# Performance work log

Measured on AMD Instinct MI355X. Metric: run time of the kernel, lower is better.

The kernel has to match this reference:

```python
import jax, jax.numpy as jnp
import numpy as np

B, S, HID = 2, 2048, 1024
H, KVH, D = 16, 4, 64
N_REP = H // KVH
SCALE = D ** -0.5
CAP = 50.0


def rotate_half(x):
    x1, x2 = x[..., : D // 2], x[..., D // 2 :]
    return jnp.concatenate((-x2, x1), axis=-1)


def setup_inputs() -> dict:
    key = jax.random.key(0)
    ks = jax.random.split(key, 10)
    X = jax.random.normal(ks[0], (B, S, HID), dtype=jnp.float32)
    # RoPE tables: (B, S, D)
    inv_freq = 1.0 / (10000.0 ** (np.arange(0, D, 2, dtype=np.float32) / D))
    pos = np.arange(S, dtype=np.float32)
    freqs = np.outer(pos, inv_freq)  # (S, D/2)
    emb = np.concatenate([freqs, freqs], axis=-1)  # (S, D)
    cos = jnp.broadcast_to(jnp.asarray(np.cos(emb)), (B, S, D))
    sin = jnp.broadcast_to(jnp.asarray(np.sin(emb)), (B, S, D))
    # causal mask: 1 where key <= query
    mask = jnp.broadcast_to(jnp.tril(jnp.ones((S, S), dtype=jnp.int32)), (B, S, S))
    std = HID ** -0.5
    Wq = jax.random.normal(ks[1], (HID, HID), dtype=jnp.float32) * std
    bq = jnp.zeros((HID,), dtype=jnp.float32)
    Wk = jax.random.normal(ks[2], (KVH * D, HID), dtype=jnp.float32) * std
    bk = jnp.zeros((KVH * D,), dtype=jnp.float32)
    Wv = jax.random.normal(ks[3], (KVH * D, HID), dtype=jnp.float32) * std
    bv = jnp.zeros((KVH * D,), dtype=jnp.float32)
    Wo = jax.random.normal(ks[4], (HID, HID), dtype=jnp.float32) * std
    bo = jnp.zeros((HID,), dtype=jnp.float32)
    return {"X": X, "cos": cos, "sin": sin, "mask": mask,
            "Wq": Wq, "bq": bq, "Wk": Wk, "bk": bk,
            "Wv": Wv, "bv": bv, "Wo": Wo, "bo": bo}


def reference(X, cos, sin, mask, Wq, bq, Wk, bk, Wv, bv, Wo, bo):
    bsz, q_len, _ = X.shape
    q = (X @ Wq.T + bq).reshape(bsz, q_len, H, D).transpose(0, 2, 1, 3)    # (B,H,S,D)
    k = (X @ Wk.T + bk).reshape(bsz, q_len, KVH, D).transpose(0, 2, 1, 3)  # (B,KVH,S,D)
    v = (X @ Wv.T + bv).reshape(bsz, q_len, KVH, D).transpose(0, 2, 1, 3)
    c = cos[:, None, :, :]  # (B,1,S,D)
    s = sin[:, None, :, :]
    q = q * c + rotate_half(q) * s
    k = k * c + rotate_half(k) * s
    k = jnp.repeat(k, N_REP, axis=1)  # GQA expand -> (B,H,S,D)
    v = jnp.repeat(v, N_REP, axis=1)
    scores = jnp.einsum('bhqd,bhkd->bhqk', q, k) * SCALE
    scores = jnp.clip(scores, -CAP, CAP)  # attention cap
    scores = jnp.where(mask[:, None, :, :] == 0, -1e9, scores)
    attn = jax.nn.softmax(scores, axis=-1)  # dropout p=0 -> identity
    ctx = jnp.einsum('bhqk,bhkd->bhqd', attn, v)
    ctx = ctx.transpose(0, 2, 1, 3).reshape(bsz, q_len, H * D)
    out = ctx @ Wo.T + bo
    return (out, attn)
```

## Files before the change

### kernel.cpp

```cpp
#include <hip/hip_runtime.h>
#include <cstdint>
#include <cstddef>

#define S_LEN   2048
#define BATCH   2
#define HID_DIM 1024
#define NHEAD   16
#define NKV     4
#define DHEAD   64
#define SCALE_F 0.125f
#define CAP_F   50.0f
#define L2E     1.44269504f

typedef unsigned short u16;
typedef __attribute__((ext_vector_type(8))) short  short8_t;
typedef __attribute__((ext_vector_type(4))) float  f32x4;
typedef __attribute__((ext_vector_type(4))) u16    u16x4;

static __device__ __forceinline__ u16 f2bf(float f) {
  uint32_t x = __builtin_bit_cast(uint32_t, f);
  x += 0x7fffu + ((x >> 16) & 1u);
  return (u16)(x >> 16);
}

static __device__ __forceinline__ void gload_lds16(const void* g, void* l) {
  __builtin_amdgcn_global_load_lds((const __attribute__((address_space(1))) void*)g,
                                   (__attribute__((address_space(3))) void*)l, 16, 0, 0);
}

static __device__ __forceinline__ float expclamp(float x) {
  float c = __builtin_amdgcn_fmed3f(x, -CAP_F, CAP_F);
  return __builtin_amdgcn_exp2f(c * L2E - CAP_F * L2E);
}

__global__ void cast_all(const float* __restrict__ X,  u16* __restrict__ xb,
                         const float* __restrict__ Wq, u16* __restrict__ wqb,
                         const float* __restrict__ Wk, u16* __restrict__ wkb,
                         const float* __restrict__ Wv, u16* __restrict__ wvb,
                         const float* __restrict__ Wo, u16* __restrict__ wob) {
  const float* src; u16* dst; int n4;
  switch (blockIdx.y) {
    case 0:  src = X;  dst = xb;  n4 = (BATCH * S_LEN * HID_DIM) / 4; break;
    case 1:  src = Wq; dst = wqb; n4 = (HID_DIM * HID_DIM) / 4;       break;
    case 2:  src = Wk; dst = wkb; n4 = (NKV * DHEAD * HID_DIM) / 4;   break;
    case 3:  src = Wv; dst = wvb; n4 = (NKV * DHEAD * HID_DIM) / 4;   break;
    default: src = Wo; dst = wob; n4 = (HID_DIM * HID_DIM) / 4;       break;
  }
  for (int i = blockIdx.x * 256 + threadIdx.x; i < n4; i += gridDim.x * 256) {
    f32x4 v = ((const f32x4*)src)[i];
    u16x4 o;
    o[0] = f2bf(v[0]); o[1] = f2bf(v[1]); o[2] = f2bf(v[2]); o[3] = f2bf(v[3]);
    ((u16x4*)dst)[i] = o;
  }
}

__global__ __launch_bounds__(256) void gemm_qkv(const u16* __restrict__ Xb,
                                                const u16* __restrict__ Wqb,
                                                const u16* __restrict__ Wkb,
                                                const u16* __restrict__ Wvb,
                                                const float* __restrict__ bq,
                                                const float* __restrict__ bk,
                                                const float* __restrict__ bv,
                                                const float* __restrict__ cosb,
                                                const float* __restrict__ sinb,
                                                u16* __restrict__ qout,
                                                u16* __restrict__ kout,
                                                u16* __restrict__ vtout) {
  __shared__ u16 As[128 * 64];
  __shared__ u16 Bs[128 * 64];
  const int tid = threadIdx.x, lane = tid & 63, wid = tid >> 6;
  const int l15 = lane & 15, lg = lane >> 4;
  const int m0 = blockIdx.x * 128, n0 = blockIdx.y * 128;
  const int wm = wid & 1, wn = wid >> 1;
  const int K = HID_DIM;

  const u16* Wp; const float* biasp; int nl, mode;
  if (n0 < 1024)      { Wp = Wqb; biasp = bq; nl = n0;        mode = 0; }
  else if (n0 < 1280) { Wp = Wkb; biasp = bk; nl = n0 - 1024; mode = 1; }
  else                { Wp = Wvb; biasp = bv; nl = n0 - 1280; mode = 2; }

  f32x4 acc[4][4];
  #pragma unroll
  for (int a = 0; a < 4; ++a)
    #pragma unroll
    for (int b2 = 0; b2 < 4; ++b2) acc[a][b2] = (f32x4){0.f, 0.f, 0.f, 0.f};

  const int srow = (lane >> 3), sg = (lane & 7);

  for (int kk = 0; kk < K; kk += 64) {
    __syncthreads();
    #pragma unroll
    for (int i = 0; i < 4; ++i) {
      const int c = wid * 4 + i;
      const int r = c * 8 + srow;
      const int g = sg ^ (r & 7);
      gload_lds16(Xb + (size_t)(m0 + r) * K + kk + g * 8, As + c * 512);
      gload_lds16(Wp + (size_t)(nl + r) * K + kk + g * 8, Bs + c * 512);
    }
    __syncthreads();
    #pragma unroll
    for (int ks = 0; ks < 2; ++ks) {
      short8_t xa[4], wb[4];
      #pragma unroll
      for (int f = 0; f < 4; ++f) {
        const int rm = wm * 64 + f * 16 + l15;
        const int rn = wn * 64 + f * 16 + l15;
        xa[f] = *(const short8_t*)(As + rm * 64 + (((ks * 4 + lg) ^ (rm & 7)) * 8));
        wb[f] = *(const short8_t*)(Bs + rn * 64 + (((ks * 4 + lg) ^ (rn & 7)) * 8));
      }
      if (mode != 2) {
        #pragma unroll
        for (int fn = 0; fn < 4; ++fn)
          #pragma unroll
          for (int fm = 0; fm < 4; ++fm)
            acc[fn][fm] = __builtin_amdgcn_mfma_f32_16x16x32_bf16(wb[fn], xa[fm], acc[fn][fm], 0, 0, 0);
      } else {
        #pragma unroll
        for (int fn = 0; fn < 4; ++fn)
          #pragma unroll
          for (int fm = 0; fm < 4; ++fm)
            acc[fn][fm] = __builtin_amdgcn_mfma_f32_16x16x32_bf16(xa[fm], wb[fn], acc[fn][fm], 0, 0, 0);
      }
    }
  }

  const int m_base = m0 + wm * 64;
  const int nlb = nl + wn * 64;

  if (mode < 2) {
    const int Nout = (mode == 0) ? HID_DIM : (NKV * DHEAD);
    u16* outb = (mode == 0) ? qout : kout;
    #pragma unroll
    for (int fm = 0; fm < 4; ++fm) {
      const int row = m_base + fm * 16 + l15;
      #pragma unroll
      for (int fn = 0; fn < 2; ++fn) {
        const int dh = fn * 16 + lg * 4;
        const f32x4 c4 = *(const f32x4*)(cosb + (size_t)row * 64 + dh);
        const f32x4 s4 = *(const f32x4*)(sinb + (size_t)row * 64 + dh);
        f32x4 x1 = acc[fn][fm]     + *(const f32x4*)(biasp + nlb + fn * 16 + lg * 4);
        f32x4 x2 = acc[fn + 2][fm] + *(const f32x4*)(biasp + nlb + (fn + 2) * 16 + lg * 4);
        f32x4 o1 = x1 * c4 - x2 * s4;
        f32x4 o2 = x2 * c4 + x1 * s4;
        u16x4 u1, u2;
        #pragma unroll
        for (int i = 0; i < 4; ++i) { u1[i] = f2bf(o1[i]); u2[i] = f2bf(o2[i]); }
        *(u16x4*)(outb + (size_t)row * Nout + nlb + fn * 16 + lg * 4)       = u1;
        *(u16x4*)(outb + (size_t)row * Nout + nlb + (fn + 2) * 16 + lg * 4) = u2;
      }
    }
  } else {
    #pragma unroll
    for (int fn = 0; fn < 4; ++fn) {
      const int d = nlb + fn * 16 + l15;
      const float bvs = biasp[d];
      #pragma unroll
      for (int fm = 0; fm < 4; ++fm) {
        const int s0 = m_base + fm * 16 + lg * 4;
        const int b_ = s0 >> 11, s_ = s0 & (S_LEN - 1);
        u16x4 o;
        #pragma unroll
        for (int i = 0; i < 4; ++i) o[i] = f2bf(acc[fn][fm][i] + bvs);
        *(u16x4*)(vtout + (size_t)(b_ * 256 + d) * S_LEN + s_) = o;
      }
    }
  }
}

__global__ __launch_bounds__(256) void gemm_out(const u16* __restrict__ A,
                                                const u16* __restrict__ W,
                                                const float* __restrict__ bias,
                                                float* __restrict__ outp) {
  __shared__ u16 As[128 * 64];
  __shared__ u16 Bs[128 * 64];
  const int tid = threadIdx.x, lane = tid & 63, wid = tid >> 6;
  const int l15 = lane & 15, lg = lane >> 4;
  const int m0 = blockIdx.x * 128, n0 = blockIdx.y * 128;
  const int wm = wid & 1, wn = wid >> 1;
  const int K = HID_DIM, N = HID_DIM;

  f32x4 acc[4][4];
  #pragma unroll
  for (int a = 0; a < 4; ++a)
    #pragma unroll
    for (int b2 = 0; b2 < 4; ++b2) acc[a][b2] = (f32x4){0.f, 0.f, 0.f, 0.f};

  const int srow = (lane >> 3), sg = (lane & 7);

  for (int kk = 0; kk < K; kk += 64) {
    __syncthreads();
    #pragma unroll
    for (int i = 0; i < 4; ++i) {
      const int c = wid * 4 + i;
      const int r = c * 8 + srow;
      const int g = sg ^ (r & 7);
      gload_lds16(A + (size_t)(m0 + r) * K + kk + g * 8, As + c * 512);
      gload_lds16(W + (size_t)(n0 + r) * K + kk + g * 8, Bs + c * 512);
    }
    __syncthreads();
    #pragma unroll
    for (int ks = 0; ks < 2; ++ks) {
      short8_t xa[4], wb[4];
      #pragma unroll
      for (int f = 0; f < 4; ++f) {
        const int rm = wm * 64 + f * 16 + l15;
        const int rn = wn * 64 + f * 16 + l15;
        xa[f] = *(const short8_t*)(As + rm * 64 + (((ks * 4 + lg) ^ (rm & 7)) * 8));
        wb[f] = *(const short8_t*)(Bs + rn * 64 + (((ks * 4 + lg) ^ (rn & 7)) * 8));
      }
      #pragma unroll
      for (int fn = 0; fn < 4; ++fn)
        #pragma unroll
        for (int fm = 0; fm < 4; ++fm)
          acc[fn][fm] = __builtin_amdgcn_mfma_f32_16x16x32_bf16(wb[fn], xa[fm], acc[fn][fm], 0, 0, 0);
    }
  }

  const int m_base = m0 + wm * 64, n_base = n0 + wn * 64;
  #pragma unroll
  for (int fn = 0; fn < 4; ++fn) {
    const int col = n_base + fn * 16 + lg * 4;
    const f32x4 bvv = *(const f32x4*)(bias + col);
    #pragma unroll
    for (int fm = 0; fm < 4; ++fm) {
      const int row = m_base + fm * 16 + l15;
      *(f32x4*)(outp + (size_t)row * N + col) = acc[fn][fm] + bvv;
    }
  }
}

__global__ __launch_bounds__(512) void attn_fused(const u16* __restrict__ qb,
                                                  const u16* __restrict__ kb,
                                                  const u16* __restrict__ vtb,
                                                  float* __restrict__ attn,
                                                  u16* __restrict__ ctxb) {
  __shared__ u16 kS[2][64 * 64];
  __shared__ u16 vS[2][64 * 64];
  __shared__ u16 pS[8][16][72];

  const int tid = threadIdx.x, lane = tid & 63, wid = tid >> 6;
  const int l15 = lane & 15, lg = lane >> 4;
  const int bh = blockIdx.x, b = bh >> 4, h = bh & 15, kvh = h >> 2;
  const int qt = (int)(gridDim.y - 1 - blockIdx.y);
  const int q0 = qt * 128;
  const int NT = 2 * qt + 2;
  const int qw = q0 + wid * 16;
  const int qrow = qw + l15;

  const u16* qp = qb + (size_t)(b * S_LEN + qrow) * HID_DIM + h * DHEAD + lg * 8;
  const short8_t qf0 = *(const short8_t*)qp;
  const short8_t qf1 = *(const short8_t*)(qp + 32);

  const u16* kbase  = kb  + (size_t)(b * S_LEN) * (NKV * DHEAD) + kvh * DHEAD;
  const u16* vtbase = vtb + (size_t)(b * NKV + kvh) * DHEAD * S_LEN;

  const int sr = tid >> 3;
  const int sg = (tid & 7) ^ (sr & 7);

  auto stageK = [&](int bi, int kv0) {
    gload_lds16(kbase + (size_t)(kv0 + sr) * (NKV * DHEAD) + sg * 8, &kS[bi][tid * 8]);
  };
  auto stageV = [&](int bi, int kv0) {
    gload_lds16(vtbase + (size_t)sr * S_LEN + kv0 + sg * 8, &vS[bi][tid * 8]);
  };

  float lsum = 0.f;
  stageK(0, 0);
  for (int t = 0; t < NT; ++t) {
    const int kv0 = t * 64;
    if (t + 1 < NT) {
      stageK((t + 1) & 1, kv0 + 64);
      asm volatile("s_waitcnt vmcnt(1)" ::: "memory");
    } else {
      asm volatile("s_waitcnt vmcnt(0)" ::: "memory");
    }
    __builtin_amdgcn_s_barrier();
    if (kv0 <= qw + 15) {
      const u16* ks = kS[t & 1];
      const bool maskc = (kv0 + 63 > qw);
      #pragma unroll
      for (int g16 = 0; g16 < 4; ++g16) {
        const int r = g16 * 16 + l15;
        short8_t ka0 = *(const short8_t*)(ks + r * 64 + ((lg ^ (r & 7)) * 8));
        short8_t ka1 = *(const short8_t*)(ks + r * 64 + (((4 + lg) ^ (r & 7)) * 8));
        f32x4 sacc = (f32x4){0.f, 0.f, 0.f, 0.f};
        sacc = __builtin_amdgcn_mfma_f32_16x16x32_bf16(ka0, qf0, sacc, 0, 0, 0);
        sacc = __builtin_amdgcn_mfma_f32_16x16x32_bf16(ka1, qf1, sacc, 0, 0, 0);
        #pragma unroll
        for (int i = 0; i < 4; ++i) {
          float e = expclamp(sacc[i] * SCALE_F);
          if (maskc) {
            const int kvi = kv0 + g16 * 16 + lg * 4 + i;
            e = (kvi <= qrow) ? e : 0.f;
          }
          lsum += e;
        }
      }
    }
    __builtin_amdgcn_s_barrier();
  }
  lsum += __shfl_xor(lsum, 16);
  lsum += __shfl_xor(lsum, 32);
  const float invl = 1.f / lsum;

  float* abase = attn + (size_t)bh * S_LEN * S_LEN;
  float* arow  = abase + (size_t)qrow * S_LEN;
  f32x4 ctx[4];
  #pragma unroll
  for (int dt = 0; dt < 4; ++dt) ctx[dt] = (f32x4){0.f, 0.f, 0.f, 0.f};

  stageK(0, 0);
  stageV(0, 0);
  for (int t = 0; t < NT; ++t) {
    const int kv0 = t * 64;
    if (t + 1 < NT) {
      stageK((t + 1) & 1, kv0 + 64);
      stageV((t + 1) & 1, kv0 + 64);
      asm volatile("s_waitcnt vmcnt(2)" ::: "memory");
    } else {
      asm volatile("s_waitcnt vmcnt(0)" ::: "memory");
    }
    __builtin_amdgcn_s_barrier();
    if (kv0 > qw + 15) {
      const f32x4 z = (f32x4){0.f, 0.f, 0.f, 0.f};
      #pragma unroll
      for (int g16 = 0; g16 < 4; ++g16)
        *(f32x4*)(arow + kv0 + g16 * 16 + lg * 4) = z;
    } else {
      const u16* ks = kS[t & 1];
      const u16* vs = vS[t & 1];
      const bool maskc = (kv0 + 63 > qw);
      #pragma unroll
      for (int g16 = 0; g16 < 4; ++g16) {
        const int r = g16 * 16 + l15;
        short8_t ka0 = *(const short8_t*)(ks + r * 64 + ((lg ^ (r & 7)) * 8));
        short8_t ka1 = *(const short8_t*)(ks + r * 64 + (((4 + lg) ^ (r & 7)) * 8));
        f32x4 sacc = (f32x4){0.f, 0.f, 0.f, 0.f};
        sacc = __builtin_amdgcn_mfma_f32_16x16x32_bf16(ka0, qf0, sacc, 0, 0, 0);
        sacc = __builtin_amdgcn_mfma_f32_16x16x32_bf16(ka1, qf1, sacc, 0, 0, 0);
        f32x4 pv; u16x4 pb;
        #pragma unroll
        for (int i = 0; i < 4; ++i) {
          float e = expclamp(sacc[i] * SCALE_F);
          if (maskc) {
            const int kvi = kv0 + g16 * 16 + lg * 4 + i;
            e = (kvi <= qrow) ? e : 0.f;
          }
          float p = e * invl;
          pv[i] = p;
          pb[i] = f2bf(p);
        }
        *(f32x4*)(arow + kv0 + g16 * 16 + lg * 4) = pv;
        *(u16x4*)&pS[wid][l15][g16 * 16 + lg * 4] = pb;
      }
      short8_t pa0 = *(const short8_t*)&pS[wid][l15][lg * 8];
      short8_t pa1 = *(const short8_t*)&pS[wid][l15][32 + lg * 8];
      #pragma unroll
      for (int dt = 0; dt < 4; ++dt) {
        const int r = dt * 16 + l15;
        short8_t bv0 = *(const short8_t*)(vs + r * 64 + ((lg ^ (r & 7)) * 8));
        short8_t bv1 = *(const short8_t*)(vs + r * 64 + (((4 + lg) ^ (r & 7)) * 8));
        ctx[dt] = __builtin_amdgcn_mfma_f32_16x16x32_bf16(bv0, pa0, ctx[dt], 0, 0, 0);
        ctx[dt] = __builtin_amdgcn_mfma_f32_16x16x32_bf16(bv1, pa1, ctx[dt], 0, 0, 0);
      }
    }
    __builtin_amdgcn_s_barrier();
  }

  #pragma unroll
  for (int dt = 0; dt < 4; ++dt) {
    u16x4 o;
    #pragma unroll
    for (int i = 0; i < 4; ++i) o[i] = f2bf(ctx[dt][i]);
    *(u16x4*)(ctxb + (size_t)(b * S_LEN + qrow) * HID_DIM + h * DHEAD + dt * 16 + lg * 4) = o;
  }

  const int zc0 = q0 + 128;
  if (zc0 < S_LEN) {
    const f32x4 z = (f32x4){0.f, 0.f, 0.f, 0.f};
    for (int r = wid; r < 128; r += 8) {
      float* rowp = abase + (size_t)(q0 + r) * S_LEN;
      for (int c = zc0 + lane * 4; c < S_LEN; c += 256)
        *(f32x4*)(rowp + c) = z;
    }
  }
}

extern "C" void kernel_launch(void* const* d_in, const int* in_sizes, int n_in,
                              void* d_out, int out_size, void* d_ws, size_t ws_size,
                              hipStream_t stream) {
  (void)in_sizes; (void)n_in; (void)out_size; (void)ws_size;
  const float* X    = (const float*)d_in[0];
  const float* cosb = (const float*)d_in[1];
  const float* sinb = (const float*)d_in[2];
  const float* Wq = (const float*)d_in[4];
  const float* bq = (const float*)d_in[5];
  const float* Wk = (const float*)d_in[6];
  const float* bk = (const float*)d_in[7];
  const float* Wv = (const float*)d_in[8];
  const float* bv = (const float*)d_in[9];
  const float* Wo = (const float*)d_in[10];
  const float* bo = (const float*)d_in[11];

  float* outp  = (float*)d_out;
  float* attnp = outp + (size_t)BATCH * S_LEN * HID_DIM;

  const int M = BATCH * S_LEN;
  u16* ws    = (u16*)d_ws;
  u16* Xb    = ws;
  u16* Wqb   = Xb  + (size_t)M * HID_DIM;
  u16* Wkb   = Wqb + (size_t)HID_DIM * HID_DIM;
  u16* Wvb   = Wkb + (size_t)NKV * DHEAD * HID_DIM;
  u16* Wob   = Wvb + (size_t)NKV * DHEAD * HID_DIM;
  u16* qbuf  = Wob + (size_t)HID_DIM * HID_DIM;
  u16* kbuf  = qbuf + (size_t)M * HID_DIM;
  u16* vtbuf = kbuf + (size_t)M * NKV * DHEAD;
  u16* ctxb  = vtbuf + (size_t)M * NKV * DHEAD;

  cast_all<<<dim3(1024, 5), 256, 0, stream>>>(X, Xb, Wq, Wqb, Wk, Wkb, Wv, Wvb, Wo, Wob);

  gemm_qkv<<<dim3(M / 128, 12), 256, 0, stream>>>(Xb, Wqb, Wkb, Wvb, bq, bk, bv,
                                                  cosb, sinb, qbuf, kbuf, vtbuf);

  attn_fused<<<dim3(BATCH * NHEAD, S_LEN / 128), 512, 0, stream>>>(qbuf, kbuf, vtbuf, attnp, ctxb);

  gemm_out<<<dim3(M / 128, HID_DIM / 128), 256, 0, stream>>>(ctxb, Wob, bo, outp);
}
```

Measured before the change: 229.7 us.

## Shrink attention tiles to 64 queries, regroup blocks by KV head, fold scale into Q

The attention kernel now uses 256-thread blocks, each covering 64 query rows, launched as a 1D grid of 1024. The grid is ordered so the four query heads sharing a KV head are adjacent, with heavy causal tiles scheduled first, to improve K/V cache reuse and load balance. Because each warp now always has work, the causal skip branches are removed. The softmax scale and log2e factor are folded into Q in the QKV GEMM epilogue, so the exp path needs only a clamp and subtract, though rounding Q to bf16 after scaling slightly changes numerics. Probability and zero-fill stores to the attention matrix use nontemporal stores, and the row sum is kept in four separate accumulators.

```diff
diff --git a/kernel.cpp b/kernel.cpp
--- a/kernel.cpp
+++ b/kernel.cpp
@@ -9,8 +9,9 @@
 #define NKV     4
 #define DHEAD   64
 #define SCALE_F 0.125f
-#define CAP_F   50.0f
 #define L2E     1.44269504f
+#define QSCALE  (SCALE_F * L2E)
+#define CAPL2   (50.0f * L2E)
 
 typedef unsigned short u16;
 typedef __attribute__((ext_vector_type(8))) short  short8_t;
@@ -28,9 +29,8 @@
                                    (__attribute__((address_space(3))) void*)l, 16, 0, 0);
 }
 
-static __device__ __forceinline__ float expclamp(float x) {
-  float c = __builtin_amdgcn_fmed3f(x, -CAP_F, CAP_F);
-  return __builtin_amdgcn_exp2f(c * L2E - CAP_F * L2E);
+static __device__ __forceinline__ float expclamp2(float x) {
+  return __builtin_amdgcn_exp2f(__builtin_amdgcn_fmed3f(x, -CAPL2, CAPL2) - CAPL2);
 }
 
 __global__ void cast_all(const float* __restrict__ X,  u16* __restrict__ xb,
@@ -129,6 +129,7 @@
 
   if (mode < 2) {
     const int Nout = (mode == 0) ? HID_DIM : (NKV * DHEAD);
+    const float qs = (mode == 0) ? QSCALE : 1.0f;
     u16* outb = (mode == 0) ? qout : kout;
     #pragma unroll
     for (int fm = 0; fm < 4; ++fm) {
@@ -140,8 +141,8 @@
         const f32x4 s4 = *(const f32x4*)(sinb + (size_t)row * 64 + dh);
         f32x4 x1 = acc[fn][fm]     + *(const f32x4*)(biasp + nlb + fn * 16 + lg * 4);
         f32x4 x2 = acc[fn + 2][fm] + *(const f32x4*)(biasp + nlb + (fn + 2) * 16 + lg * 4);
-        f32x4 o1 = x1 * c4 - x2 * s4;
-        f32x4 o2 = x2 * c4 + x1 * s4;
+        f32x4 o1 = (x1 * c4 - x2 * s4) * qs;
+        f32x4 o2 = (x2 * c4 + x1 * s4) * qs;
         u16x4 u1, u2;
         #pragma unroll
         for (int i = 0; i < 4; ++i) { u1[i] = f2bf(o1[i]); u2[i] = f2bf(o2[i]); }
@@ -229,21 +230,28 @@
   }
 }
 
-__global__ __launch_bounds__(512) void attn_fused(const u16* __restrict__ qb,
+__global__ __launch_bounds__(256) void attn_fused(const u16* __restrict__ qb,
                                                   const u16* __restrict__ kb,
                                                   const u16* __restrict__ vtb,
                                                   float* __restrict__ attn,
                                                   u16* __restrict__ ctxb) {
   __shared__ u16 kS[2][64 * 64];
   __shared__ u16 vS[2][64 * 64];
-  __shared__ u16 pS[8][16][72];
+  __shared__ u16 pS[4][16][72];
 
   const int tid = threadIdx.x, lane = tid & 63, wid = tid >> 6;
   const int l15 = lane & 15, lg = lane >> 4;
-  const int bh = blockIdx.x, b = bh >> 4, h = bh & 15, kvh = h >> 2;
-  const int qt = (int)(gridDim.y - 1 - blockIdx.y);
-  const int q0 = qt * 128;
-  const int NT = 2 * qt + 2;
+
+  const int lin = blockIdx.x;
+  const int g8  = lin & 7;
+  const int rem = lin >> 3;
+  const int h2  = rem & 3;
+  const int qt  = 31 - (rem >> 2);
+  const int b   = g8 >> 2, kvh = g8 & 3, h = kvh * 4 + h2;
+  const int bh  = b * 16 + h;
+
+  const int q0 = qt * 64;
+  const int NT = qt + 1;
   const int qw = q0 + wid * 16;
   const int qrow = qw + l15;
 
@@ -254,51 +262,62 @@
   const u16* kbase  = kb  + (size_t)(b * S_LEN) * (NKV * DHEAD) + kvh * DHEAD;
   const u16* vtbase = vtb + (size_t)(b * NKV + kvh) * DHEAD * S_LEN;
 
-  const int sr = tid >> 3;
-  const int sg = (tid & 7) ^ (sr & 7);
+  const int sr8 = wid * 8 + (lane >> 3);
+  const int sgr = lane & 7;
 
   auto stageK = [&](int bi, int kv0) {
-    gload_lds16(kbase + (size_t)(kv0 + sr) * (NKV * DHEAD) + sg * 8, &kS[bi][tid * 8]);
+    #pragma unroll
+    for (int it = 0; it < 2; ++it) {
+      const int r = it * 32 + sr8;
+      const int g = sgr ^ (r & 7);
+      gload_lds16(kbase + (size_t)(kv0 + r) * (NKV * DHEAD) + g * 8,
+                  &kS[bi][(it * 32 + wid * 8) * 64]);
+    }
   };
   auto stageV = [&](int bi, int kv0) {
-    gload_lds16(vtbase + (size_t)sr * S_LEN + kv0 + sg * 8, &vS[bi][tid * 8]);
+    #pragma unroll
+    for (int it = 0; it < 2; ++it) {
+      const int r = it * 32 + sr8;
+      const int g = sgr ^ (r & 7);
+      gload_lds16(vtbase + (size_t)r * S_LEN + kv0 + g * 8,
+                  &vS[bi][(it * 32 + wid * 8) * 64]);
+    }
   };
 
-  float lsum = 0.f;
+  f32x4 lacc = (f32x4){0.f, 0.f, 0.f, 0.f};
   stageK(0, 0);
   for (int t = 0; t < NT; ++t) {
     const int kv0 = t * 64;
     if (t + 1 < NT) {
       stageK((t + 1) & 1, kv0 + 64);
-      asm volatile("s_waitcnt vmcnt(1)" ::: "memory");
+      asm volatile("s_waitcnt vmcnt(2)" ::: "memory");
     } else {
       asm volatile("s_waitcnt vmcnt(0)" ::: "memory");
     }
     __builtin_amdgcn_s_barrier();
-    if (kv0 <= qw + 15) {
-      const u16* ks = kS[t & 1];
-      const bool maskc = (kv0 + 63 > qw);
-      #pragma unroll
-      for (int g16 = 0; g16 < 4; ++g16) {
-        const int r = g16 * 16 + l15;
-        short8_t ka0 = *(const short8_t*)(ks + r * 64 + ((lg ^ (r & 7)) * 8));
-        short8_t ka1 = *(const short8_t*)(ks + r * 64 + (((4 + lg) ^ (r & 7)) * 8));
-        f32x4 sacc = (f32x4){0.f, 0.f, 0.f, 0.f};
-        sacc = __builtin_amdgcn_mfma_f32_16x16x32_bf16(ka0, qf0, sacc, 0, 0, 0);
-        sacc = __builtin_amdgcn_mfma_f32_16x16x32_bf16(ka1, qf1, sacc, 0, 0, 0);
-        #pragma unroll
-        for (int i = 0; i < 4; ++i) {
-          float e = expclamp(sacc[i] * SCALE_F);
-          if (maskc) {
-            const int kvi = kv0 + g16 * 16 + lg * 4 + i;
-            e = (kvi <= qrow) ? e : 0.f;
-          }
-          lsum += e;
+    const u16* ks = kS[t & 1];
+    const bool maskc = (kv0 + 63 > qw);
+    #pragma unroll
+    for (int g16 = 0; g16 < 4; ++g16) {
+      const int r = g16 * 16 + l15;
+      short8_t ka0 = *(const short8_t*)(ks + r * 64 + ((lg ^ (r & 7)) * 8));
+      short8_t ka1 = *(const short8_t*)(ks + r * 64 + (((4 + lg) ^ (r & 7)) * 8));
+      f32x4 sacc = (f32x4){0.f, 0.f, 0.f, 0.f};
+      sacc = __builtin_amdgcn_mfma_f32_16x16x32_bf16(ka0, qf0, sacc, 0, 0, 0);
+      sacc = __builtin_amdgcn_mfma_f32_16x16x32_bf16(ka1, qf1, sacc, 0, 0, 0);
+      #pragma unroll
+      for (int i = 0; i < 4; ++i) {
+        float e = expclamp2(sacc[i]);
+        if (maskc) {
+          const int kvi = kv0 + g16 * 16 + lg * 4 + i;
+          e = (kvi <= qrow) ? e : 0.f;
         }
+        lacc[i] += e;
       }
     }
     __builtin_amdgcn_s_barrier();
   }
+  float lsum = (lacc[0] + lacc[1]) + (lacc[2] + lacc[3]);
   lsum += __shfl_xor(lsum, 16);
   lsum += __shfl_xor(lsum, 32);
   const float invl = 1.f / lsum;
@@ -316,53 +335,46 @@
     if (t + 1 < NT) {
       stageK((t + 1) & 1, kv0 + 64);
       stageV((t + 1) & 1, kv0 + 64);
-      asm volatile("s_waitcnt vmcnt(2)" ::: "memory");
+      asm volatile("s_waitcnt vmcnt(4)" ::: "memory");
     } else {
       asm volatile("s_waitcnt vmcnt(0)" ::: "memory");
     }
     __builtin_amdgcn_s_barrier();
-    if (kv0 > qw + 15) {
-      const f32x4 z = (f32x4){0.f, 0.f, 0.f, 0.f};
-      #pragma unroll
-      for (int g16 = 0; g16 < 4; ++g16)
-        *(f32x4*)(arow + kv0 + g16 * 16 + lg * 4) = z;
-    } else {
-      const u16* ks = kS[t & 1];
-      const u16* vs = vS[t & 1];
-      const bool maskc = (kv0 + 63 > qw);
-      #pragma unroll
-      for (int g16 = 0; g16 < 4; ++g16) {
-        const int r = g16 * 16 + l15;
-        short8_t ka0 = *(const short8_t*)(ks + r * 64 + ((lg ^ (r & 7)) * 8));
-        short8_t ka1 = *(const short8_t*)(ks + r * 64 + (((4 + lg) ^ (r & 7)) * 8));
-        f32x4 sacc = (f32x4){0.f, 0.f, 0.f, 0.f};
-        sacc = __builtin_amdgcn_mfma_f32_16x16x32_bf16(ka0, qf0, sacc, 0, 0, 0);
-        sacc = __builtin_amdgcn_mfma_f32_16x16x32_bf16(ka1, qf1, sacc, 0, 0, 0);
-        f32x4 pv; u16x4 pb;
-        #pragma unroll
-        for (int i = 0; i < 4; ++i) {
-          float e = expclamp(sacc[i] * SCALE_F);
-          if (maskc) {
-            const int kvi = kv0 + g16 * 16 + lg * 4 + i;
-            e = (kvi <= qrow) ? e : 0.f;
-          }
-          float p = e * invl;
-          pv[i] = p;
-          pb[i] = f2bf(p);
+    const u16* ks = kS[t & 1];
+    const u16* vs = vS[t & 1];
+    const bool maskc = (kv0 + 63 > qw);
+    #pragma unroll
+    for (int g16 = 0; g16 < 4; ++g16) {
+      const int r = g16 * 16 + l15;
+      short8_t ka0 = *(const short8_t*)(ks + r * 64 + ((lg ^ (r & 7)) * 8));
+      short8_t ka1 = *(const short8_t*)(ks + r * 64 + (((4 + lg) ^ (r & 7)) * 8));
+      f32x4 sacc = (f32x4){0.f, 0.f, 0.f, 0.f};
+      sacc = __builtin_amdgcn_mfma_f32_16x16x32_bf16(ka0, qf0, sacc, 0, 0, 0);
+      sacc = __builtin_amdgcn_mfma_f32_16x16x32_bf16(ka1, qf1, sacc, 0, 0, 0);
+      f32x4 pv; u16x4 pb;
+      #pragma unroll
+      for (int i = 0; i < 4; ++i) {
+        float e = expclamp2(sacc[i]);
+        if (maskc) {
+          const int kvi = kv0 + g16 * 16 + lg * 4 + i;
+          e = (kvi <= qrow) ? e : 0.f;
         }
-        *(f32x4*)(arow + kv0 + g16 * 16 + lg * 4) = pv;
-        *(u16x4*)&pS[wid][l15][g16 * 16 + lg * 4] = pb;
-      }
-      short8_t pa0 = *(const short8_t*)&pS[wid][l15][lg * 8];
-      short8_t pa1 = *(const short8_t*)&pS[wid][l15][32 + lg * 8];
-      #pragma unroll
-      for (int dt = 0; dt < 4; ++dt) {
-        const int r = dt * 16 + l15;
-        short8_t bv0 = *(const short8_t*)(vs + r * 64 + ((lg ^ (r & 7)) * 8));
-        short8_t bv1 = *(const short8_t*)(vs + r * 64 + (((4 + lg) ^ (r & 7)) * 8));
-        ctx[dt] = __builtin_amdgcn_mfma_f32_16x16x32_bf16(bv0, pa0, ctx[dt], 0, 0, 0);
-        ctx[dt] = __builtin_amdgcn_mfma_f32_16x16x32_bf16(bv1, pa1, ctx[dt], 0, 0, 0);
-      }
+        float p = e * invl;
+        pv[i] = p;
+        pb[i] = f2bf(p);
+      }
+      __builtin_nontemporal_store(pv, (f32x4*)(arow + kv0 + g16 * 16 + lg * 4));
+      *(u16x4*)&pS[wid][l15][g16 * 16 + lg * 4] = pb;
+    }
+    short8_t pa0 = *(const short8_t*)&pS[wid][l15][lg * 8];
+    short8_t pa1 = *(const short8_t*)&pS[wid][l15][32 + lg * 8];
+    #pragma unroll
+    for (int dt = 0; dt < 4; ++dt) {
+      const int r = dt * 16 + l15;
+      short8_t bv0 = *(const short8_t*)(vs + r * 64 + ((lg ^ (r & 7)) * 8));
+      short8_t bv1 = *(const short8_t*)(vs + r * 64 + (((4 + lg) ^ (r & 7)) * 8));
+      ctx[dt] = __builtin_amdgcn_mfma_f32_16x16x32_bf16(bv0, pa0, ctx[dt], 0, 0, 0);
+      ctx[dt] = __builtin_amdgcn_mfma_f32_16x16x32_bf16(bv1, pa1, ctx[dt], 0, 0, 0);
     }
     __builtin_amdgcn_s_barrier();
   }
@@ -375,13 +387,13 @@
     *(u16x4*)(ctxb + (size_t)(b * S_LEN + qrow) * HID_DIM + h * DHEAD + dt * 16 + lg * 4) = o;
   }
 
-  const int zc0 = q0 + 128;
+  const int zc0 = q0 + 64;
   if (zc0 < S_LEN) {
     const f32x4 z = (f32x4){0.f, 0.f, 0.f, 0.f};
-    for (int r = wid; r < 128; r += 8) {
+    for (int r = wid; r < 64; r += 4) {
       float* rowp = abase + (size_t)(q0 + r) * S_LEN;
       for (int c = zc0 + lane * 4; c < S_LEN; c += 256)
-        *(f32x4*)(rowp + c) = z;
+        __builtin_nontemporal_store(z, (f32x4*)(rowp + c));
     }
   }
 }
@@ -422,7 +434,7 @@
   gemm_qkv<<<dim3(M / 128, 12), 256, 0, stream>>>(Xb, Wqb, Wkb, Wvb, bq, bk, bv,
                                                   cosb, sinb, qbuf, kbuf, vtbuf);
 
-  attn_fused<<<dim3(BATCH * NHEAD, S_LEN / 128), 512, 0, stream>>>(qbuf, kbuf, vtbuf, attnp, ctxb);
+  attn_fused<<<dim3(1024), 256, 0, stream>>>(qbuf, kbuf, vtbuf, attnp, ctxb);
 
   gemm_out<<<dim3(M / 128, HID_DIM / 128), 256, 0, stream>>>(ctxb, Wob, bo, outp);
 }
```

After: 281.1 us. 22.4% more time.
